# Optimization experiments

Measured on AMD Instinct MI355X. Metric: run time of the kernel, lower is better.

The kernel has to match this reference:

```python
import jax, jax.numpy as jnp
import numpy as np

RADIUS = 0.1
NUM_POINT = 1024  # M centroids
SAMPLE_NUM = 32   # K neighbors per ball


def fps(xyz, m):
    """D-FPS farthest point sampling. xyz: (B,N,3) -> idx (B,m) int32."""
    B, N, _ = xyz.shape

    def step(carry, _):
        mind, far = carry  # mind (B,N), far (B,)
        centroid = jnp.take_along_axis(xyz, far[:, None, None], axis=1)  # (B,1,3)
        d = jnp.sum((xyz - centroid) ** 2, axis=-1)  # (B,N)
        mind = jnp.minimum(mind, d)
        nxt = jnp.argmax(mind, axis=1).astype(jnp.int32)
        return (mind, nxt), far

    init = (jnp.full((B, N), jnp.inf, xyz.dtype), jnp.zeros((B,), jnp.int32))
    _, idx = jax.lax.scan(step, init, None, length=m)
    return jnp.transpose(idx)  # (B,m)


def ball_query(new_xyz, xyz, radius, k):
    """First-k points within radius of each centroid, padded with first hit.
    new_xyz (B,M,3), xyz (B,N,3) -> (B,M,k) int32."""
    N = xyz.shape[1]
    d2 = jnp.sum((new_xyz[:, :, None, :] - xyz[:, None, :, :]) ** 2, axis=-1)  # (B,M,N)
    order = jnp.where(d2 < radius * radius, jnp.arange(N, dtype=jnp.int32)[None, None, :], N)
    neg, pos = jax.lax.top_k(-order, k)  # k smallest 'order' values -> first-k in-ball indices
    valid = (-neg) < N
    return jnp.where(valid, pos, pos[..., :1])


def setup_inputs() -> dict:
    key = jax.random.key(0)
    ks = jax.random.split(key, 12)
    B, N, C = 4, 16384, 64
    Cin = C + 3  # use_xyz=True
    points_xyz = jax.random.uniform(ks[0], (B, N, 3), dtype=jnp.float32)
    features = jax.random.normal(ks[1], (B, C, N), dtype=jnp.float32)
    s = lambda fan: 1.0 / np.sqrt(fan)
    inp = {
        "points_xyz": points_xyz,
        "features": features,
        "Wa": jax.random.normal(ks[2], (128, Cin), jnp.float32) * s(Cin),
        "ba": jnp.zeros((128,), jnp.float32),
        "Wb": jax.random.normal(ks[3], (128, 128), jnp.float32) * s(128),
        "bb": jnp.zeros((128,), jnp.float32),
        "Ws": jax.random.normal(ks[4], (128, Cin), jnp.float32) * s(Cin),
        "bs": jnp.zeros((128,), jnp.float32),
        "Wc": jax.random.normal(ks[5], (512, 128), jnp.float32) * s(128),
        "bc": jnp.zeros((512,), jnp.float32),
        "Wd": jax.random.normal(ks[6], (128, 512), jnp.float32) * s(512),
        "bd": jnp.zeros((128,), jnp.float32),
    }
    return inp


def _conv1x1(W, b, x):
    # pointwise conv over (B,C,M,K)
    return jnp.einsum('oc,bcmk->bomk', W, x) + b[None, :, None, None]


def reference(points_xyz, features, Wa, ba, Wb, bb, Ws, bs, Wc, bc, Wd, bd):
    idx = fps(points_xyz, NUM_POINT)  # (B,M)
    new_xyz = jnp.take_along_axis(points_xyz, idx[:, :, None], axis=1)  # (B,M,3)
    nidx = ball_query(new_xyz, points_xyz, RADIUS, SAMPLE_NUM)  # (B,M,K)
    # gather and relativize grouped xyz; gather grouped features
    grouped_xyz = jax.vmap(lambda p, i: p[i])(points_xyz, nidx) - new_xyz[:, :, None, :]  # (B,M,K,3)
    gfeat = jax.vmap(lambda f, i: f[:, i])(features, nidx)  # (B,C,M,K)
    g = jnp.concatenate([jnp.transpose(grouped_xyz, (0, 3, 1, 2)), gfeat], axis=1)  # (B,3+C,M,K)
    # mlp + shortcut residual + relu
    h = _conv1x1(Wb, bb, jax.nn.relu(_conv1x1(Wa, ba, g)))
    h = jax.nn.relu(h + _conv1x1(Ws, bs, g))
    # inverted mlp + identity residual + relu
    inv = _conv1x1(Wd, bd, jax.nn.relu(_conv1x1(Wc, bc, h)))
    out = jax.nn.relu(inv + h)
    pooled = jnp.max(out, axis=-1)  # max pool over K -> (B,128,M)
    return new_xyz, pooled, idx
```

## Files before the change

kernel.cpp:

```cpp
#include <hip/hip_runtime.h>

#define N_PTS   16384
#define M_CENT  1024
#define K_SMP   32
#define C_FEAT  64
#define NCELL   512

using bf16x8 = __attribute__((ext_vector_type(8))) short;
using s16x4  = __attribute__((ext_vector_type(4))) short;
using f32x4  = __attribute__((ext_vector_type(4))) float;

__device__ inline short f2bf(float f) {
    unsigned u = __float_as_uint(f);
    u += 0x7fffu + ((u >> 16) & 1u);
    return (short)(u >> 16);
}

__device__ inline int part3(int v) {
    return (v & 1) | ((v & 2) << 2) | ((v & 4) << 4);
}
__device__ inline int cell_of(float x, float y, float z) {
    int xi = (int)(x * 8.0f); xi = xi < 0 ? 0 : (xi > 7 ? 7 : xi);
    int yi = (int)(y * 8.0f); yi = yi < 0 ? 0 : (yi > 7 ? 7 : yi);
    int zi = (int)(z * 8.0f); zi = zi < 0 ? 0 : (zi > 7 ? 7 : zi);
    return part3(xi) | (part3(yi) << 1) | (part3(zi) << 2);
}

__global__ __launch_bounds__(1024) void hist_kernel(
    const float* __restrict__ xyz, int* __restrict__ ghist)
{
    __shared__ int h[NCELL];
    const int b = blockIdx.x, tid = threadIdx.x;
    if (tid < NCELL) h[tid] = 0;
    __syncthreads();
    const float* P = xyz + (size_t)b * N_PTS * 3;
    for (int i = 0; i < 16; ++i) {
        const int p = tid + (i << 10);
        atomicAdd(&h[cell_of(P[p*3], P[p*3+1], P[p*3+2])], 1);
    }
    __syncthreads();
    if (tid < NCELL) ghist[b * NCELL + tid] = h[tid];
}

__global__ __launch_bounds__(NCELL) void scan_kernel(
    const int* __restrict__ ghist, int* __restrict__ gbase)
{
    __shared__ int h[NCELL];
    const int b = blockIdx.x, t = threadIdx.x;
    h[t] = ghist[b * NCELL + t];
    __syncthreads();
    int s = 0;
    for (int i = 0; i < t; ++i) s += h[i];
    gbase[b * NCELL + t] = s;
}

__global__ __launch_bounds__(1024) void scatter_kernel(
    const float* __restrict__ xyz, int* __restrict__ gbase,
    float4* __restrict__ gsxyz)
{
    const int b = blockIdx.x, tid = threadIdx.x;
    const float* P = xyz + (size_t)b * N_PTS * 3;
    for (int i = 0; i < 16; ++i) {
        const int p = tid + (i << 10);
        float x = P[p*3], y = P[p*3+1], z = P[p*3+2];
        int c = cell_of(x, y, z);
        int pos = atomicAdd(&gbase[b * NCELL + c], 1);
        gsxyz[(size_t)b * N_PTS + pos] = make_float4(x, y, z, __int_as_float(p));
    }
}

__global__ __launch_bounds__(1024) void fps_kernel(
    const float* __restrict__ xyz,
    const float4* __restrict__ gsxyz,
    float* __restrict__ newxyz_out,
    float* __restrict__ idxf_out)
{
#pragma clang fp contract(off)
    const int b = blockIdx.x, tid = threadIdx.x;
    const int wid = tid >> 6, lane = tid & 63;
    const float4* S = gsxyz + (size_t)b * N_PTS;

    float px[16], py[16], pz[16], mind[16];
    unsigned klo[16];
    float lox = 1e30f, hix = -1e30f, loy = 1e30f, hiy = -1e30f, loz = 1e30f, hiz = -1e30f;
#pragma unroll
    for (int i = 0; i < 16; ++i) {
        const float4 v = S[tid * 16 + i];
        px[i] = v.x; py[i] = v.y; pz[i] = v.z;
        const int orig = __float_as_int(v.w);
        klo[i] = ((unsigned)(16383 - orig) << 16) | (unsigned)(tid * 16 + i);
        mind[i] = __int_as_float(0x7f800000);
        lox = fminf(lox, v.x); hix = fmaxf(hix, v.x);
        loy = fminf(loy, v.y); hiy = fmaxf(hiy, v.y);
        loz = fminf(loz, v.z); hiz = fmaxf(hiz, v.z);
    }
    float wlx = lox, whx = hix, wly = loy, why = hiy, wlz = loz, whz = hiz;
#pragma unroll
    for (int off = 1; off < 64; off <<= 1) {
        wlx = fminf(wlx, __shfl_xor(wlx, off)); whx = fmaxf(whx, __shfl_xor(whx, off));
        wly = fminf(wly, __shfl_xor(wly, off)); why = fmaxf(why, __shfl_xor(why, off));
        wlz = fminf(wlz, __shfl_xor(wlz, off)); whz = fmaxf(whz, __shfl_xor(whz, off));
    }

    __shared__ unsigned long long wslot[M_CENT];
    __shared__ unsigned long long wbest[16];
    wslot[tid] = 0ull;
    if (tid < 16) wbest[tid] = 0ull;

    const float* P = xyz + (size_t)b * N_PTS * 3;
    float cx = P[0], cy = P[1], cz = P[2];
    if (tid == 0) {
        idxf_out[b * M_CENT] = 0.0f;
        newxyz_out[(b * M_CENT) * 3 + 0] = cx;
        newxyz_out[(b * M_CENT) * 3 + 1] = cy;
        newxyz_out[(b * M_CENT) * 3 + 2] = cz;
    }
    __syncthreads();

    unsigned long long bkey = 0x7f80000000000000ull;
    unsigned long long wkey = 0x7f80000000000000ull;

    for (int j = 1; j < M_CENT; ++j) {
        float twx = fmaxf(fmaxf(wlx - cx, cx - whx), 0.0f);
        float twy = fmaxf(fmaxf(wly - cy, cy - why), 0.0f);
        float twz = fmaxf(fmaxf(wlz - cz, cz - whz), 0.0f);
        float wlb = (twx * twx + twy * twy) + twz * twz;
        float wmax = __uint_as_float((unsigned)(wkey >> 32));
        if (wlb * 0.999985f < wmax) {
            float tx = fmaxf(fmaxf(lox - cx, cx - hix), 0.0f);
            float ty = fmaxf(fmaxf(loy - cy, cy - hiy), 0.0f);
            float tz = fmaxf(fmaxf(loz - cz, cz - hiz), 0.0f);
            float lb = (tx * tx + ty * ty) + tz * tz;
            float lmax = __uint_as_float((unsigned)(bkey >> 32));
            bool need = (lb * 0.999985f) < lmax;
            if (__any(need)) {
                unsigned long long best = 0ull;
#pragma unroll
                for (int i = 0; i < 16; ++i) {
                    float dx = px[i] - cx;
                    float dy = py[i] - cy;
                    float dz = pz[i] - cz;
                    float xx = dx * dx, yy = dy * dy, zz = dz * dz;
                    float d  = (xx + yy) + zz;
                    float mn = fminf(mind[i], d);
                    mind[i] = mn;
                    unsigned long long cand =
                        ((unsigned long long)__float_as_uint(mn) << 32) | klo[i];
                    if (cand > best) best = cand;
                }
                bkey = best;
                atomicMax(&wbest[wid], best);
                unsigned long long nw = wbest[wid];
                wkey = nw;
                if (lane == 0) wbest[wid] = 0ull;
            }
        }
        if (lane == 0) atomicMax(&wslot[j], wkey);
        __syncthreads();

        const unsigned long long wk = wslot[j];
        const unsigned int kl = (unsigned int)wk;
        const int sorted = (int)(kl & 0xFFFFu);
        const float4 wv = S[sorted];
        cx = wv.x; cy = wv.y; cz = wv.z;
        if (tid == 0) {
            const int orig = 16383 - (int)(kl >> 16);
            idxf_out[b * M_CENT + j] = (float)orig;
            newxyz_out[(b * M_CENT + j) * 3 + 0] = cx;
            newxyz_out[(b * M_CENT + j) * 3 + 1] = cy;
            newxyz_out[(b * M_CENT + j) * 3 + 2] = cz;
        }
    }
}

__global__ __launch_bounds__(256) void ball_kernel(
    const float* __restrict__ xyz,
    const float* __restrict__ newxyz,
    int* __restrict__ nidx)
{
#pragma clang fp contract(off)
    const float R2 = (float)(0.1 * 0.1);
    const int gw   = blockIdx.x * 4 + (threadIdx.x >> 6);
    const int lane = threadIdx.x & 63;
    const int b    = gw >> 10;
    const float* P = xyz + (size_t)b * N_PTS * 3;
    const float cx = newxyz[gw * 3 + 0];
    const float cy = newxyz[gw * 3 + 1];
    const float cz = newxyz[gw * 3 + 2];
    int* out = nidx + gw * K_SMP;

    int cnt = 0, first = -1;
    for (int base = 0; base < N_PTS; base += 64) {
        const int n = base + lane;
        float dx = P[n * 3 + 0] - cx;
        float dy = P[n * 3 + 1] - cy;
        float dz = P[n * 3 + 2] - cz;
        float xx = dx * dx, yy = dy * dy, zz = dz * dz;
        float d2 = (xx + yy) + zz;
        bool inb = d2 < R2;
        unsigned long long mask = __ballot(inb);
        if (mask) {
            if (first < 0) first = base + __ffsll(mask) - 1;
            int before = __popcll(mask & ((1ull << lane) - 1ull));
            int slot = cnt + before;
            if (inb && slot < K_SMP) out[slot] = n;
            cnt += __popcll(mask);
            if (cnt >= K_SMP) break;
        }
    }
    for (int s = cnt + lane; s < K_SMP; s += 64) out[s] = first;
}

__global__ void prep_w(const float* __restrict__ src, short* __restrict__ dst,
                       int OC, int IC, int ICP, int remap)
{
    int i = blockIdx.x * 256 + threadIdx.x;
    if (i >= OC * ICP) return;
    int oc = i / ICP, ic = i - oc * ICP;
    float v = 0.0f;
    if (remap) {
        if (ic < 64)      v = src[oc * IC + 3 + ic];
        else if (ic < 67) v = src[oc * IC + (ic - 64)];
    } else if (ic < IC)   v = src[oc * IC + ic];
    dst[i] = f2bf(v);
}

__global__ __launch_bounds__(256) void tfeat_kernel(
    const float* __restrict__ feat, float* __restrict__ featT)
{
    __shared__ float t[64][65];
    const int b = blockIdx.y;
    const int n0 = blockIdx.x * 64;
    for (int it = 0; it < 16; ++it) {
        int idx = it * 256 + threadIdx.x;
        int c = idx >> 6, n = idx & 63;
        t[c][n] = feat[((size_t)b * 64 + c) * N_PTS + n0 + n];
    }
    __syncthreads();
    for (int it = 0; it < 16; ++it) {
        int idx = it * 256 + threadIdx.x;
        int n = idx >> 6, c = idx & 63;
        featT[((size_t)b * N_PTS + n0 + n) * 64 + c] = t[c][n];
    }
}

__global__ __launch_bounds__(256, 2) void mlp_kernel(
    const float* __restrict__ xyz, const float* __restrict__ feat,
    const float* __restrict__ featT, int useT,
    const float* __restrict__ newxyz, const int* __restrict__ nidx,
    const short* __restrict__ WaB, const float* __restrict__ ba,
    const short* __restrict__ WbB, const float* __restrict__ bb,
    const short* __restrict__ WsB, const float* __restrict__ bs,
    const short* __restrict__ WcB, const float* __restrict__ bc,
    const short* __restrict__ WdB, const float* __restrict__ bd,
    float* __restrict__ pooled)
{
    __shared__ short Xt[64][104];
    __shared__ short Ht[64][136];
    __shared__ short Tt[64][136];

    const int tid = threadIdx.x;
    const int w = tid >> 6, l = tid & 63, l16 = l & 15, kg = l >> 4;
    const int cen0 = blockIdx.x * 2;
    const int b = cen0 >> 10;
    const int ocw = 32 * w;

    {
        const int col = tid >> 2, part = tid & 3;
        const int ci = cen0 + (col >> 5);
        const int nn = nidx[ci * K_SMP + (col & 31)];
        float v[16];
        if (useT) {
            const f32x4* src = (const f32x4*)(featT + ((size_t)b * N_PTS + nn) * 64 + part * 16);
            f32x4 f0 = src[0], f1 = src[1], f2 = src[2], f3 = src[3];
            v[0]=f0[0]; v[1]=f0[1]; v[2]=f0[2]; v[3]=f0[3];
            v[4]=f1[0]; v[5]=f1[1]; v[6]=f1[2]; v[7]=f1[3];
            v[8]=f2[0]; v[9]=f2[1]; v[10]=f2[2]; v[11]=f2[3];
            v[12]=f3[0]; v[13]=f3[1]; v[14]=f3[2]; v[15]=f3[3];
        } else {
            const float* F = feat + (size_t)b * C_FEAT * N_PTS + nn;
#pragma unroll
            for (int q = 0; q < 16; ++q) v[q] = F[(size_t)(part * 16 + q) * N_PTS];
        }
        bf16x8 h0, h1;
#pragma unroll
        for (int q = 0; q < 8; ++q) { h0[q] = f2bf(v[q]); h1[q] = f2bf(v[q + 8]); }
        *(bf16x8*)&Xt[col][part * 16]     = h0;
        *(bf16x8*)&Xt[col][part * 16 + 8] = h1;
        if (part == 0) {
            bf16x8 hx, z;
#pragma unroll
            for (int q = 0; q < 8; ++q) { hx[q] = 0; z[q] = 0; }
            hx[0] = f2bf(xyz[((size_t)b * N_PTS + nn) * 3 + 0] - newxyz[ci * 3 + 0]);
            hx[1] = f2bf(xyz[((size_t)b * N_PTS + nn) * 3 + 1] - newxyz[ci * 3 + 1]);
            hx[2] = f2bf(xyz[((size_t)b * N_PTS + nn) * 3 + 2] - newxyz[ci * 3 + 2]);
            *(bf16x8*)&Xt[col][64] = hx;
            *(bf16x8*)&Xt[col][72] = z;
            *(bf16x8*)&Xt[col][80] = z;
            *(bf16x8*)&Xt[col][88] = z;
        }
    }
    __syncthreads();

    f32x4 accA[2][4], accS[2][4];
#pragma unroll
    for (int o = 0; o < 2; ++o)
#pragma unroll
        for (int ct = 0; ct < 4; ++ct) {
#pragma unroll
            for (int r = 0; r < 4; ++r) { accA[o][ct][r] = 0.f; accS[o][ct][r] = 0.f; }
        }
#pragma unroll
    for (int k = 0; k < 3; ++k) {
        bf16x8 xb[4];
#pragma unroll
        for (int ct = 0; ct < 4; ++ct)
            xb[ct] = *(const bf16x8*)&Xt[ct * 16 + l16][k * 32 + kg * 8];
#pragma unroll
        for (int o = 0; o < 2; ++o) {
            const int row = ocw + o * 16 + l16;
            bf16x8 wa  = *(const bf16x8*)(WaB + row * 96 + k * 32 + kg * 8);
            bf16x8 wsv = *(const bf16x8*)(WsB + row * 96 + k * 32 + kg * 8);
#pragma unroll
            for (int ct = 0; ct < 4; ++ct) {
                accA[o][ct] = __builtin_amdgcn_mfma_f32_16x16x32_bf16(wa,  xb[ct], accA[o][ct], 0, 0, 0);
                accS[o][ct] = __builtin_amdgcn_mfma_f32_16x16x32_bf16(wsv, xb[ct], accS[o][ct], 0, 0, 0);
            }
        }
    }
#pragma unroll
    for (int o = 0; o < 2; ++o) {
        const f32x4 bav = *(const f32x4*)(ba + ocw + o * 16 + kg * 4);
#pragma unroll
        for (int ct = 0; ct < 4; ++ct) {
            s16x4 hv;
#pragma unroll
            for (int r = 0; r < 4; ++r) hv[r] = f2bf(fmaxf(accA[o][ct][r] + bav[r], 0.f));
            *(s16x4*)&Ht[ct * 16 + l16][ocw + o * 16 + kg * 4] = hv;
        }
    }
    __syncthreads();

    f32x4 accB[2][4];
#pragma unroll
    for (int o = 0; o < 2; ++o)
#pragma unroll
        for (int ct = 0; ct < 4; ++ct) {
#pragma unroll
            for (int r = 0; r < 4; ++r) accB[o][ct][r] = 0.f;
        }
#pragma unroll
    for (int k = 0; k < 4; ++k) {
        bf16x8 xb[4];
#pragma unroll
        for (int ct = 0; ct < 4; ++ct)
            xb[ct] = *(const bf16x8*)&Ht[ct * 16 + l16][k * 32 + kg * 8];
#pragma unroll
        for (int o = 0; o < 2; ++o) {
            const int row = ocw + o * 16 + l16;
            bf16x8 wbv = *(const bf16x8*)(WbB + row * 128 + k * 32 + kg * 8);
#pragma unroll
            for (int ct = 0; ct < 4; ++ct)
                accB[o][ct] = __builtin_amdgcn_mfma_f32_16x16x32_bf16(wbv, xb[ct], accB[o][ct], 0, 0, 0);
        }
    }
    f32x4 hreg[2][4];
#pragma unroll
    for (int o = 0; o < 2; ++o) {
        const f32x4 bbv = *(const f32x4*)(bb + ocw + o * 16 + kg * 4);
        const f32x4 bsv = *(const f32x4*)(bs + ocw + o * 16 + kg * 4);
#pragma unroll
        for (int ct = 0; ct < 4; ++ct) {
#pragma unroll
            for (int r = 0; r < 4; ++r)
                hreg[o][ct][r] = fmaxf((accB[o][ct][r] + bbv[r]) + (accS[o][ct][r] + bsv[r]), 0.f);
        }
    }
    __syncthreads();
#pragma unroll
    for (int o = 0; o < 2; ++o)
#pragma unroll
        for (int ct = 0; ct < 4; ++ct) {
            s16x4 hv;
#pragma unroll
            for (int r = 0; r < 4; ++r) hv[r] = f2bf(hreg[o][ct][r]);
            *(s16x4*)&Ht[ct * 16 + l16][ocw + o * 16 + kg * 4] = hv;
        }
    __syncthreads();

    f32x4 accD[2][4];
#pragma unroll
    for (int o = 0; o < 2; ++o)
#pragma unroll
        for (int ct = 0; ct < 4; ++ct) {
#pragma unroll
            for (int r = 0; r < 4; ++r) accD[o][ct][r] = 0.f;
        }
    for (int cc = 0; cc < 4; ++cc) {
        f32x4 accC[2][4];
#pragma unroll
        for (int o = 0; o < 2; ++o)
#pragma unroll
            for (int ct = 0; ct < 4; ++ct) {
#pragma unroll
                for (int r = 0; r < 4; ++r) accC[o][ct][r] = 0.f;
            }
#pragma unroll
        for (int k = 0; k < 4; ++k) {
            bf16x8 xb[4];
#pragma unroll
            for (int ct = 0; ct < 4; ++ct)
                xb[ct] = *(const bf16x8*)&Ht[ct * 16 + l16][k * 32 + kg * 8];
#pragma unroll
            for (int o = 0; o < 2; ++o) {
                const int row = cc * 128 + ocw + o * 16 + l16;
                bf16x8 wcv = *(const bf16x8*)(WcB + row * 128 + k * 32 + kg * 8);
#pragma unroll
                for (int ct = 0; ct < 4; ++ct)
                    accC[o][ct] = __builtin_amdgcn_mfma_f32_16x16x32_bf16(wcv, xb[ct], accC[o][ct], 0, 0, 0);
            }
        }
        __syncthreads();
#pragma unroll
        for (int o = 0; o < 2; ++o) {
            const f32x4 bcv = *(const f32x4*)(bc + cc * 128 + ocw + o * 16 + kg * 4);
#pragma unroll
            for (int ct = 0; ct < 4; ++ct) {
                s16x4 tv;
#pragma unroll
                for (int r = 0; r < 4; ++r) tv[r] = f2bf(fmaxf(accC[o][ct][r] + bcv[r], 0.f));
                *(s16x4*)&Tt[ct * 16 + l16][ocw + o * 16 + kg * 4] = tv;
            }
        }
        __syncthreads();
#pragma unroll
        for (int k = 0; k < 4; ++k) {
            bf16x8 tb[4];
#pragma unroll
            for (int ct = 0; ct < 4; ++ct)
                tb[ct] = *(const bf16x8*)&Tt[ct * 16 + l16][k * 32 + kg * 8];
#pragma unroll
            for (int o = 0; o < 2; ++o) {
                const int row = ocw + o * 16 + l16;
                bf16x8 wdv = *(const bf16x8*)(WdB + row * 512 + cc * 128 + k * 32 + kg * 8);
#pragma unroll
                for (int ct = 0; ct < 4; ++ct)
                    accD[o][ct] = __builtin_amdgcn_mfma_f32_16x16x32_bf16(wdv, tb[ct], accD[o][ct], 0, 0, 0);
            }
        }
    }

    const int m0 = cen0 & 1023;
#pragma unroll
    for (int o = 0; o < 2; ++o) {
        const f32x4 bdv = *(const f32x4*)(bd + ocw + o * 16 + kg * 4);
#pragma unroll
        for (int r = 0; r < 4; ++r) {
            float a0 = fmaxf((accD[o][0][r] + bdv[r]) + hreg[o][0][r], 0.f);
            float a1 = fmaxf((accD[o][1][r] + bdv[r]) + hreg[o][1][r], 0.f);
            float a2 = fmaxf((accD[o][2][r] + bdv[r]) + hreg[o][2][r], 0.f);
            float a3 = fmaxf((accD[o][3][r] + bdv[r]) + hreg[o][3][r], 0.f);
            float u0 = fmaxf(a0, a1), u1 = fmaxf(a2, a3);
#pragma unroll
            for (int off = 1; off < 16; off <<= 1) {
                u0 = fmaxf(u0, __shfl_xor(u0, off));
                u1 = fmaxf(u1, __shfl_xor(u1, off));
            }
            if (l16 == 0) {
                const int oc = ocw + o * 16 + kg * 4 + r;
                pooled[((size_t)b * 128 + oc) * 1024 + m0]     = u0;
                pooled[((size_t)b * 128 + oc) * 1024 + m0 + 1] = u1;
            }
        }
    }
}

extern "C" void kernel_launch(void* const* d_in, const int* in_sizes, int n_in,
                              void* d_out, int out_size, void* d_ws, size_t ws_size,
                              hipStream_t stream)
{
    const float* xyz  = (const float*)d_in[0];
    const float* feat = (const float*)d_in[1];
    const float* Wa = (const float*)d_in[2];   const float* ba = (const float*)d_in[3];
    const float* Wb = (const float*)d_in[4];   const float* bb = (const float*)d_in[5];
    const float* Ws = (const float*)d_in[6];   const float* bs = (const float*)d_in[7];
    const float* Wc = (const float*)d_in[8];   const float* bc = (const float*)d_in[9];
    const float* Wd = (const float*)d_in[10];  const float* bd = (const float*)d_in[11];

    float* out    = (float*)d_out;
    float* newxyz = out;
    float* pooled = out + 4 * 1024 * 3;
    float* idxf   = pooled + 4 * 128 * 1024;

    char* ws = (char*)d_ws;
    float4* gsxyz = (float4*)ws;
    int*    nidx  = (int*)ws;
    short* WaB = (short*)(ws + (1 << 20));
    short* WsB = WaB + 128 * 96;
    short* WbB = WsB + 128 * 96;
    short* WcB = WbB + 128 * 128;
    short* WdB = WcB + 512 * 128;
    int*   ghist = (int*)(WdB + 128 * 512);
    int*   gbase = ghist + 4 * NCELL;
    float* featT = (float*)(ws + (2 << 20));

    const size_t need = (size_t)(2 << 20) + (size_t)4 * N_PTS * 64 * 4;
    const int useT = (ws_size >= need) ? 1 : 0;

    prep_w<<<(128 *  96 + 255) / 256, 256, 0, stream>>>(Wa, WaB, 128,  67,  96, 1);
    prep_w<<<(128 *  96 + 255) / 256, 256, 0, stream>>>(Ws, WsB, 128,  67,  96, 1);
    prep_w<<<(128 * 128 + 255) / 256, 256, 0, stream>>>(Wb, WbB, 128, 128, 128, 0);
    prep_w<<<(512 * 128 + 255) / 256, 256, 0, stream>>>(Wc, WcB, 512, 128, 128, 0);
    prep_w<<<(128 * 512 + 255) / 256, 256, 0, stream>>>(Wd, WdB, 128, 512, 512, 0);
    if (useT) tfeat_kernel<<<dim3(N_PTS / 64, 4), 256, 0, stream>>>(feat, featT);

    hist_kernel   <<<4, 1024,  0, stream>>>(xyz, ghist);
    scan_kernel   <<<4, NCELL, 0, stream>>>(ghist, gbase);
    scatter_kernel<<<4, 1024,  0, stream>>>(xyz, gbase, gsxyz);

    fps_kernel<<<4, 1024, 0, stream>>>(xyz, gsxyz, newxyz, idxf);
    ball_kernel<<<1024, 256, 0, stream>>>(xyz, newxyz, nidx);
    mlp_kernel<<<2048, 256, 0, stream>>>(xyz, feat, featT, useT, newxyz, nidx,
                                         WaB, ba, WbB, bb, WsB, bs,
                                         WcB, bc, WdB, bd, pooled);
}
```

Measured before the change: 1.606 ms.

## Replace LDS atomic argmax in FPS with shuffle reductions and double-buffered slots

The FPS loop drops the per-wave LDS atomicMax and the per-iteration block atomic slot array. Each wave now reduces its argmax key with 64-bit xor shuffles and writes it to a parity double-buffered shared array, and every wave then reduces the 16 wave keys with shuffles. The per-thread argmax is split into a float max followed by a key select, and the wave-level bounding-box skip test is removed. The intent is to cut LDS atomic traffic and serialization on the single-block sequential critical path, at the cost of more shuffle instructions and losing the coarse wave-level early skip.

```diff
diff --git a/kernel.cpp b/kernel.cpp
--- a/kernel.cpp
+++ b/kernel.cpp
@@ -14,6 +14,14 @@
     unsigned u = __float_as_uint(f);
     u += 0x7fffu + ((u >> 16) & 1u);
     return (short)(u >> 16);
+}
+
+__device__ inline unsigned long long shfl_xor_u64(unsigned long long v, int m) {
+    int lo = (int)(unsigned int)v;
+    int hi = (int)(unsigned int)(v >> 32);
+    lo = __shfl_xor(lo, m);
+    hi = __shfl_xor(hi, m);
+    return ((unsigned long long)(unsigned int)hi << 32) | (unsigned int)lo;
 }
 
 __device__ inline int part3(int v) {
@@ -94,18 +102,8 @@
         loy = fminf(loy, v.y); hiy = fmaxf(hiy, v.y);
         loz = fminf(loz, v.z); hiz = fmaxf(hiz, v.z);
     }
-    float wlx = lox, whx = hix, wly = loy, why = hiy, wlz = loz, whz = hiz;
-#pragma unroll
-    for (int off = 1; off < 64; off <<= 1) {
-        wlx = fminf(wlx, __shfl_xor(wlx, off)); whx = fmaxf(whx, __shfl_xor(whx, off));
-        wly = fminf(wly, __shfl_xor(wly, off)); why = fmaxf(why, __shfl_xor(why, off));
-        wlz = fminf(wlz, __shfl_xor(wlz, off)); whz = fmaxf(whz, __shfl_xor(whz, off));
-    }
-
-    __shared__ unsigned long long wslot[M_CENT];
-    __shared__ unsigned long long wbest[16];
-    wslot[tid] = 0ull;
-    if (tid < 16) wbest[tid] = 0ull;
+
+    __shared__ unsigned long long wblk[2][16];
 
     const float* P = xyz + (size_t)b * N_PTS * 3;
     float cx = P[0], cy = P[1], cz = P[2];
@@ -121,45 +119,51 @@
     unsigned long long wkey = 0x7f80000000000000ull;
 
     for (int j = 1; j < M_CENT; ++j) {
-        float twx = fmaxf(fmaxf(wlx - cx, cx - whx), 0.0f);
-        float twy = fmaxf(fmaxf(wly - cy, cy - why), 0.0f);
-        float twz = fmaxf(fmaxf(wlz - cz, cz - whz), 0.0f);
-        float wlb = (twx * twx + twy * twy) + twz * twz;
-        float wmax = __uint_as_float((unsigned)(wkey >> 32));
-        if (wlb * 0.999985f < wmax) {
-            float tx = fmaxf(fmaxf(lox - cx, cx - hix), 0.0f);
-            float ty = fmaxf(fmaxf(loy - cy, cy - hiy), 0.0f);
-            float tz = fmaxf(fmaxf(loz - cz, cz - hiz), 0.0f);
-            float lb = (tx * tx + ty * ty) + tz * tz;
-            float lmax = __uint_as_float((unsigned)(bkey >> 32));
-            bool need = (lb * 0.999985f) < lmax;
-            if (__any(need)) {
-                unsigned long long best = 0ull;
-#pragma unroll
-                for (int i = 0; i < 16; ++i) {
-                    float dx = px[i] - cx;
-                    float dy = py[i] - cy;
-                    float dz = pz[i] - cz;
-                    float xx = dx * dx, yy = dy * dy, zz = dz * dz;
-                    float d  = (xx + yy) + zz;
-                    float mn = fminf(mind[i], d);
-                    mind[i] = mn;
-                    unsigned long long cand =
-                        ((unsigned long long)__float_as_uint(mn) << 32) | klo[i];
-                    if (cand > best) best = cand;
-                }
-                bkey = best;
-                atomicMax(&wbest[wid], best);
-                unsigned long long nw = wbest[wid];
-                wkey = nw;
-                if (lane == 0) wbest[wid] = 0ull;
-            }
-        }
-        if (lane == 0) atomicMax(&wslot[j], wkey);
+        const int par = j & 1;
+        float tx = fmaxf(fmaxf(lox - cx, cx - hix), 0.0f);
+        float ty = fmaxf(fmaxf(loy - cy, cy - hiy), 0.0f);
+        float tz = fmaxf(fmaxf(loz - cz, cz - hiz), 0.0f);
+        float lb = (tx * tx + ty * ty) + tz * tz;
+        float lmax = __uint_as_float((unsigned)(bkey >> 32));
+        bool need = (lb * 0.999985f) < lmax;
+
+        if (__any(need)) {
+            float bv = -1.0f;
+#pragma unroll
+            for (int i = 0; i < 16; ++i) {
+                float dx = px[i] - cx;
+                float dy = py[i] - cy;
+                float dz = pz[i] - cz;
+                float xx = dx * dx, yy = dy * dy, zz = dz * dz;
+                float d  = (xx + yy) + zz;
+                float mn = fminf(mind[i], d);
+                mind[i] = mn;
+                bv = fmaxf(bv, mn);
+            }
+            unsigned bk = 0u;
+#pragma unroll
+            for (int i = 0; i < 16; ++i)
+                if (mind[i] == bv && klo[i] > bk) bk = klo[i];
+            bkey = ((unsigned long long)__float_as_uint(bv) << 32) | bk;
+
+            unsigned long long w = bkey;
+#pragma unroll
+            for (int off = 32; off >= 1; off >>= 1) {
+                unsigned long long o = shfl_xor_u64(w, off);
+                if (o > w) w = o;
+            }
+            wkey = w;
+        }
+        if (lane == 0) wblk[par][wid] = wkey;
         __syncthreads();
 
-        const unsigned long long wk = wslot[j];
-        const unsigned int kl = (unsigned int)wk;
+        unsigned long long k2 = wblk[par][lane & 15];
+#pragma unroll
+        for (int off = 8; off >= 1; off >>= 1) {
+            unsigned long long o = shfl_xor_u64(k2, off);
+            if (o > k2) k2 = o;
+        }
+        const unsigned int kl = (unsigned int)k2;
         const int sorted = (int)(kl & 0xFFFFu);
         const float4 wv = S[sorted];
         cx = wv.x; cy = wv.y; cz = wv.z;
```

Result: no change. 1.591 ms (-0.9%).
